# Optimization experiments

Measured on AMD Instinct MI355X. Metric: run time of the kernel, lower is better.

Reference implementation:

```python
import jax, jax.numpy as jnp
import numpy as np

HID = 256
HEADS = 8
DPH = HID // HEADS  # 32
N = 65536
E = 262144


def _ln(x, g, b):
    m = jnp.mean(x, axis=-1, keepdims=True)
    v = jnp.var(x, axis=-1, keepdims=True)
    return (x - m) * jax.lax.rsqrt(v + 1e-5) * g + b


def _gelu(x):
    return jax.nn.gelu(x, approximate=False)


def _mlp2(x, W1, b1, W2, b2, act):
    return act(x @ W1 + b1) @ W2 + b2


def setup_inputs() -> dict:
    key = jax.random.key(0)
    ks = jax.random.split(key, 32)
    d = {}
    d["x"] = jax.random.normal(ks[0], (N, HID), jnp.float32)
    d["edge_index"] = jax.random.randint(ks[1], (2, E), 0, N, dtype=jnp.int32)
    d["edge_attr"] = jax.random.normal(ks[2], (E, 7), jnp.float32)
    i = 3
    def p(shape, s=0.02):
        nonlocal i
        out = jax.random.normal(ks[i], shape, jnp.float32) * s
        i += 1
        return out
    for nm, (din, dh, do) in [("q", (2 * HID + 3, 2 * HID, HID)),
                              ("k", (2 * HID + 3, 2 * HID, HID)),
                              ("v", (2 * HID + 3, 2 * HID, HID)),
                              ("s", (4, 64, HEADS)),
                              ("f", (HID, 2 * HID, HID))]:
        d[nm + "W1"] = p((din, dh))
        d[nm + "b1"] = jnp.zeros((dh,), jnp.float32)
        d[nm + "W2"] = p((dh, do))
        d[nm + "b2"] = jnp.zeros((do,), jnp.float32)
    d["ln_g"] = jnp.ones((HID,), jnp.float32)
    d["ln_b"] = jnp.zeros((HID,), jnp.float32)
    d["rW"] = p((2 * HID, HID))
    d["rb"] = jnp.zeros((HID,), jnp.float32)
    return d


def reference(x, edge_index, edge_attr,
              qW1, qb1, qW2, qb2,
              kW1, kb1, kW2, kb2,
              vW1, vb1, vW2, vb2,
              sW1, sb1, sW2, sb2,
              ln_g, ln_b, rW, rb,
              fW1, fb1, fW2, fb2):
    n_nodes = x.shape[0]
    original_x = x
    residual = x
    xn = _ln(x, ln_g, ln_b)

    src = edge_index[0]
    dst = edge_index[1]
    # gather endpoint features, concat with molecular edge feats -> [E, 2*HID+3]
    comb = jnp.concatenate([xn[src], xn[dst], edge_attr[:, :3]], axis=1)

    Q = _mlp2(comb, qW1, qb1, qW2, qb2, _gelu).reshape(-1, HEADS, DPH)
    K = _mlp2(comb, kW1, kb1, kW2, kb2, _gelu).reshape(-1, HEADS, DPH)
    V = _mlp2(comb, vW1, vb1, vW2, vb2, _gelu).reshape(-1, HEADS, DPH)

    scale = jnp.sqrt(jnp.float32(DPH))
    scores = jnp.einsum('ehd,egd->ehg', Q, K) / scale  # [E, H, H]
    bias = _mlp2(edge_attr[:, 3:7], sW1, sb1, sW2, sb2, jax.nn.relu)[:, :, None]  # [E, H, 1]
    attn = jax.nn.softmax(scores + bias, axis=1)  # softmax over dim=1, as in torch code
    wv = jnp.einsum('ehg,egd->ehd', attn, V).reshape(-1, HID)  # [E, HID]

    # scatter-mean to target nodes (edge_index[1])
    sums = jax.ops.segment_sum(wv, dst, num_segments=n_nodes)
    cnt = jax.ops.segment_sum(jnp.ones((wv.shape[0],), wv.dtype), dst, num_segments=n_nodes)
    out = sums / jnp.maximum(cnt, 1.0)[:, None]

    x1 = residual + out
    fused = jnp.concatenate([x1, original_x], axis=-1)
    x2 = x1 + (fused @ rW + rb)
    x3 = x2 + _mlp2(_ln(x2, ln_g, ln_b), fW1, fb1, fW2, fb2, _gelu)
    return x3
```

## Files before the change

kernel.cpp:

```cpp
#include <hip/hip_runtime.h>

#define N_NODES 65536
#define N_EDGES 262144

typedef unsigned short u16;
typedef unsigned char u8;
typedef float f32x4 __attribute__((ext_vector_type(4)));
typedef _Float16 h2 __attribute__((ext_vector_type(2)));
typedef _Float16 v8h __attribute__((ext_vector_type(8)));

__device__ __forceinline__ u16 f2h(float f) {
  return __builtin_bit_cast(u16, (_Float16)f);
}
__device__ __forceinline__ u8 f2e5m2(float f) {
  _Float16 h = (_Float16)f;
  u16 hb = __builtin_bit_cast(u16, h);
  hb = (u16)(hb + 0x7F + ((hb >> 8) & 1));
  return (u8)(hb >> 8);
}
__device__ __forceinline__ void dec4(unsigned d, float* o) {
  o[0] = (float)__builtin_bit_cast(_Float16, (u16)((d << 8) & 0xFF00u));
  o[1] = (float)__builtin_bit_cast(_Float16, (u16)(d & 0xFF00u));
  o[2] = (float)__builtin_bit_cast(_Float16, (u16)((d >> 8) & 0xFF00u));
  o[3] = (float)__builtin_bit_cast(_Float16, (u16)((d >> 16) & 0xFF00u));
}
__device__ __forceinline__ h2 e5lo(unsigned d) {
  return __builtin_bit_cast(h2, __builtin_amdgcn_perm(d, 0u, 0x05000400u));
}
__device__ __forceinline__ h2 e5hi(unsigned d) {
  return __builtin_bit_cast(h2, __builtin_amdgcn_perm(d, 0u, 0x07000600u));
}
__device__ __forceinline__ float gelu_s(float x) {
  float e = __expf(1.702f * x);
  return x - __fdividef(x, e + 1.0f);
}
__device__ __forceinline__ float gelu_f(float x) {
  float y = 1.5957691216057308f * (x + 0.044715f * x * x * x);
  float e = __expf(y);
  return x - __fdividef(x, e + 1.0f);
}
__device__ __forceinline__ void gld16(const u16* g, u16* l) {
  __builtin_amdgcn_global_load_lds(
      (const __attribute__((address_space(1))) void*)g,
      (__attribute__((address_space(3))) void*)l, 16, 0, 0);
}

__global__ __launch_bounds__(256) void ln_kernel(const float* __restrict__ x,
                                                 const float* __restrict__ g,
                                                 const float* __restrict__ b,
                                                 u16* __restrict__ out) {
  int row = blockIdx.x * 4 + (threadIdx.x >> 6);
  int lane = threadIdx.x & 63;
  float4 v = ((const float4*)(x + (size_t)row * 256))[lane];
  float s = v.x + v.y + v.z + v.w;
  float s2 = v.x * v.x + v.y * v.y + v.z * v.z + v.w * v.w;
#pragma unroll
  for (int off = 1; off < 64; off <<= 1) {
    s += __shfl_xor(s, off, 64);
    s2 += __shfl_xor(s2, off, 64);
  }
  float mean = s * (1.0f / 256.0f);
  float var = s2 * (1.0f / 256.0f) - mean * mean;
  float rs = rsqrtf(var + 1e-5f);
  float4 gv = ((const float4*)g)[lane];
  float4 bv = ((const float4*)b)[lane];
  ushort4 o;
  o.x = f2h((v.x - mean) * rs * gv.x + bv.x);
  o.y = f2h((v.y - mean) * rs * gv.y + bv.y);
  o.z = f2h((v.z - mean) * rs * gv.z + bv.z);
  o.w = f2h((v.w - mean) * rs * gv.w + bv.w);
  *(ushort4*)(out + (size_t)row * 256 + lane * 4) = o;
}

template <typename Epi>
__global__ __launch_bounds__(256) void gemm_bt(const u16* __restrict__ A,
                                               const u16* __restrict__ BT,
                                               int K, Epi epi) {
  __shared__ __align__(16) u16 sA[128 * 48];
  __shared__ __align__(16) u16 sB[128 * 48];
  const int tm = blockIdx.x * 128, tn = blockIdx.y * 128;
  const int t = threadIdx.x;
  const int wave = t >> 6, lane = t & 63;
  const int lrow = lane & 15, quad = lane >> 4;
  const int wrow = (wave & 1) * 64, wcol = (wave >> 1) * 64;
  const int r = t >> 2, c = (t & 3) << 3;
  f32x4 acc[4][4];
  const f32x4 z = {0.f, 0.f, 0.f, 0.f};
#pragma unroll
  for (int i = 0; i < 4; ++i)
#pragma unroll
    for (int j = 0; j < 4; ++j) acc[i][j] = z;
  for (int k0 = 0; k0 < K; k0 += 32) {
    *(uint4*)&sA[r * 48 + c] = *(const uint4*)&A[(size_t)(tm + r) * K + k0 + c];
    *(uint4*)&sA[(r + 64) * 48 + c] = *(const uint4*)&A[(size_t)(tm + r + 64) * K + k0 + c];
    *(uint4*)&sB[r * 48 + c] = *(const uint4*)&BT[(size_t)(tn + r) * K + k0 + c];
    *(uint4*)&sB[(r + 64) * 48 + c] = *(const uint4*)&BT[(size_t)(tn + r + 64) * K + k0 + c];
    __syncthreads();
    v8h af[4], bfv[4];
#pragma unroll
    for (int i = 0; i < 4; ++i) af[i] = *(const v8h*)&sA[(wrow + i * 16 + lrow) * 48 + quad * 8];
#pragma unroll
    for (int j = 0; j < 4; ++j) bfv[j] = *(const v8h*)&sB[(wcol + j * 16 + lrow) * 48 + quad * 8];
#pragma unroll
    for (int i = 0; i < 4; ++i)
#pragma unroll
      for (int j = 0; j < 4; ++j)
        acc[i][j] = __builtin_amdgcn_mfma_f32_16x16x32_f16(af[i], bfv[j], acc[i][j], 0, 0, 0);
    __syncthreads();
  }
#pragma unroll
  for (int i = 0; i < 4; ++i)
#pragma unroll
    for (int j = 0; j < 4; ++j)
#pragma unroll
      for (int rg = 0; rg < 4; ++rg)
        epi(tm + wrow + i * 16 + quad * 4 + rg, tn + wcol + j * 16 + lrow, acc[i][j][rg]);
}

#define GEMM_DBUF(K_)                                                                    \
  const int t = threadIdx.x;                                                             \
  const int wave = t >> 6, lane = t & 63;                                                \
  const int lrow = lane & 15, quad = lane >> 4;                                          \
  const int wrow = (wave & 1) * 64, wcol = (wave >> 1) * 64;                             \
  const int sa0 = 2 * wave, sa1 = 2 * wave + 1;                                          \
  const u16* pa0 = A + (size_t)(tm + sa0 * 16 + lrow) * (K_) + quad * 8;                 \
  const u16* pa1 = A + (size_t)(tm + sa1 * 16 + lrow) * (K_) + quad * 8;                 \
  const u16* pb0 = BT + (size_t)(tn + sa0 * 16 + lrow) * (K_) + quad * 8;                \
  const u16* pb1 = BT + (size_t)(tn + sa1 * 16 + lrow) * (K_) + quad * 8;                \
  f32x4 acc[4][4];                                                                       \
  {                                                                                      \
    const f32x4 z = {0.f, 0.f, 0.f, 0.f};                                                \
    _Pragma("unroll") for (int i = 0; i < 4; ++i)                                        \
        _Pragma("unroll") for (int j = 0; j < 4; ++j) acc[i][j] = z;                     \
  }                                                                                      \
  gld16(pa0, &sAB[sa0 * 512]);                                                           \
  gld16(pa1, &sAB[sa1 * 512]);                                                           \
  gld16(pb0, &sAB[4096 + sa0 * 512]);                                                    \
  gld16(pb1, &sAB[4096 + sa1 * 512]);                                                    \
  pa0 += 32; pa1 += 32; pb0 += 32; pb1 += 32;                                            \
  __syncthreads();                                                                       \
  int cur = 0;                                                                           \
  _Pragma("unroll") for (int k0 = 32; k0 < (K_); k0 += 32) {                             \
    const int nxt = cur ^ 1;                                                             \
    gld16(pa0, &sAB[nxt * 8192 + sa0 * 512]);                                            \
    gld16(pa1, &sAB[nxt * 8192 + sa1 * 512]);                                            \
    gld16(pb0, &sAB[nxt * 8192 + 4096 + sa0 * 512]);                                     \
    gld16(pb1, &sAB[nxt * 8192 + 4096 + sa1 * 512]);                                     \
    pa0 += 32; pa1 += 32; pb0 += 32; pb1 += 32;                                          \
    v8h af[4], bfv[4];                                                                   \
    _Pragma("unroll") for (int i = 0; i < 4; ++i) af[i] =                                \
        *(const v8h*)&sAB[cur * 8192 + ((wave & 1) * 4 + i) * 512 + lane * 8];           \
    _Pragma("unroll") for (int j = 0; j < 4; ++j) bfv[j] =                               \
        *(const v8h*)&sAB[cur * 8192 + 4096 + ((wave >> 1) * 4 + j) * 512 + lane * 8];   \
    _Pragma("unroll") for (int i = 0; i < 4; ++i)                                        \
        _Pragma("unroll") for (int j = 0; j < 4; ++j) acc[i][j] =                        \
            __builtin_amdgcn_mfma_f32_16x16x32_f16(af[i], bfv[j], acc[i][j], 0, 0, 0);   \
    __syncthreads();                                                                     \
    cur = nxt;                                                                           \
  }                                                                                      \
  {                                                                                      \
    v8h af[4], bfv[4];                                                                   \
    _Pragma("unroll") for (int i = 0; i < 4; ++i) af[i] =                                \
        *(const v8h*)&sAB[cur * 8192 + ((wave & 1) * 4 + i) * 512 + lane * 8];           \
    _Pragma("unroll") for (int j = 0; j < 4; ++j) bfv[j] =                               \
        *(const v8h*)&sAB[cur * 8192 + 4096 + ((wave >> 1) * 4 + j) * 512 + lane * 8];   \
    _Pragma("unroll") for (int i = 0; i < 4; ++i)                                        \
        _Pragma("unroll") for (int j = 0; j < 4; ++j) acc[i][j] =                        \
            __builtin_amdgcn_mfma_f32_16x16x32_f16(af[i], bfv[j], acc[i][j], 0, 0, 0);   \
  }

__global__ __launch_bounds__(256) void gemm2_ab(const u16* __restrict__ A,
                                                const u16* __restrict__ BT,
                                                const float* __restrict__ b1cat,
                                                u8* __restrict__ out) {
  __shared__ __align__(16) u16 sAB[16384];
  const int bid = blockIdx.x;
  const int local = bid >> 3;
  const int mt = (bid & 7) * 64 + local / 24;
  const int nt = local % 24;
  const int tm = mt * 128, tn = nt * 128;
  GEMM_DBUF(256)
  __syncthreads();
  float bj[4];
#pragma unroll
  for (int j = 0; j < 4; ++j)
    bj[j] = (nt < 12) ? b1cat[tn + wcol + j * 16 + lrow] : 0.f;
  u8* sb = (u8*)sAB;
#pragma unroll
  for (int i = 0; i < 4; ++i)
#pragma unroll
    for (int j = 0; j < 4; ++j)
#pragma unroll
      for (int rg = 0; rg < 4; ++rg)
        sb[(wrow + i * 16 + quad * 4 + rg) * 136 + wcol + j * 16 + lrow] =
            f2e5m2(acc[i][j][rg] + bj[j]);
  __syncthreads();
  {
    int ir = t >> 1, sg = t & 1;
    const u8* srcp = &sb[ir * 136 + sg * 64];
    uint2* dstp = (uint2*)(out + (size_t)(tm + ir) * 3072 + tn + sg * 64);
#pragma unroll
    for (int q = 0; q < 8; ++q) dstp[q] = *(const uint2*)(srcp + q * 8);
  }
}

struct EpiX2 {
  float* x2;
  const float* x1;
  const float* rb;
  __device__ void operator()(int m, int n, float v) const {
    x2[(size_t)m * 256 + n] = v + rb[n] + x1[(size_t)m * 256 + n];
  }
};
struct EpiHf {
  u16* hf;
  const float* b1;
  __device__ void operator()(int m, int n, float v) const {
    hf[(size_t)m * 512 + n] = f2h(gelu_f(v + b1[n]));
  }
};
struct EpiOut {
  float* out;
  const float* b2;
  const float* x2;
  __device__ void operator()(int m, int n, float v) const {
    out[(size_t)m * 256 + n] = v + b2[n] + x2[(size_t)m * 256 + n];
  }
};

__global__ void prep_w1catT(u16* __restrict__ out, const float* __restrict__ qW1,
                            const float* __restrict__ kW1, const float* __restrict__ vW1) {
  int cIdx = blockIdx.x;
  int rIdx = threadIdx.x;
  int sec = cIdx >> 9;
  int h = cIdx & 511;
  int mlp = sec % 3;
  const float* W1 = (mlp == 0) ? qW1 : (mlp == 1) ? kW1 : vW1;
  int rowoff = (sec < 3) ? 0 : 256;
  out[(size_t)cIdx * 256 + rIdx] = f2h(W1[(size_t)(rowoff + rIdx) * 512 + h]);
}
__global__ void prep_w2T(u16* __restrict__ out, const float* __restrict__ qW2,
                         const float* __restrict__ kW2, const float* __restrict__ vW2) {
  int row = blockIdx.x;
  int m = row >> 8, n = row & 255;
  const float* W2 = (m == 0) ? qW2 : (m == 1) ? kW2 : vW2;
  for (int k = threadIdx.x; k < 512; k += 256)
    out[(size_t)row * 512 + k] = f2h(W2[(size_t)k * 256 + n]);
}
__global__ void transpose_cast(u16* __restrict__ out, const float* __restrict__ in, int K, int Nn) {
  int n = blockIdx.x;
  for (int k = threadIdx.x; k < K; k += blockDim.x)
    out[(size_t)n * K + k] = f2h(in[(size_t)k * Nn + n]);
}
__global__ void prep_w1e16(u16* __restrict__ out, const float* __restrict__ qW1,
                           const float* __restrict__ kW1, const float* __restrict__ vW1) {
  int b = blockIdx.x;
  int m = b / 3, r = b % 3;
  const float* W1 = (m == 0) ? qW1 : (m == 1) ? kW1 : vW1;
  out[(size_t)b * 512 + threadIdx.x] = f2h(W1[(size_t)(512 + r) * 512 + threadIdx.x]);
}
__global__ void prep_b1cat(float* __restrict__ out, const float* __restrict__ qb1,
                           const float* __restrict__ kb1, const float* __restrict__ vb1) {
  int idx = blockIdx.x * 256 + threadIdx.x;
  const float* b = (idx < 512) ? qb1 : (idx < 1024) ? kb1 : vb1;
  out[idx] = b[idx & 511];
}

__global__ __launch_bounds__(256) void bias_kernel(const float* __restrict__ eattr,
                                                   const float* __restrict__ sW1,
                                                   const float* __restrict__ sb1,
                                                   const float* __restrict__ sW2,
                                                   const float* __restrict__ sb2,
                                                   float* __restrict__ biasb) {
  int e = blockIdx.x * 256 + threadIdx.x;
  const float* ea = eattr + (size_t)e * 7;
  float a0 = ea[3], a1 = ea[4], a2 = ea[5], a3 = ea[6];
  float acc[8];
#pragma unroll
  for (int h = 0; h < 8; ++h) acc[h] = sb2[h];
#pragma unroll 4
  for (int j = 0; j < 64; ++j) {
    float zz = fmaxf(a0 * sW1[j] + a1 * sW1[64 + j] + a2 * sW1[128 + j] + a3 * sW1[192 + j] + sb1[j], 0.f);
#pragma unroll
    for (int h = 0; h < 8; ++h) acc[h] += zz * sW2[j * 8 + h];
  }
  float4* bp = (float4*)(biasb + (size_t)e * 8);
  float4 v0 = {acc[0], acc[1], acc[2], acc[3]};
  float4 v1 = {acc[4], acc[5], acc[6], acc[7]};
  bp[0] = v0;
  bp[1] = v1;
}

__global__ __launch_bounds__(256) void hist_kernel(const int* __restrict__ dst,
                                                   unsigned* __restrict__ cnt) {
  int e = blockIdx.x * 256 + threadIdx.x;
  atomicAdd(&cnt[dst[e]], 1u);
}
__global__ __launch_bounds__(1024) void scan_kernel(const unsigned* __restrict__ cnt,
                                                    unsigned* __restrict__ off,
                                                    unsigned* __restrict__ woff) {
  __shared__ unsigned s_part[1024];
  int t = threadIdx.x;
  unsigned local[64];
  unsigned run = 0;
  const uint4* cp = (const uint4*)(cnt + t * 64);
#pragma unroll
  for (int j = 0; j < 16; ++j) {
    uint4 v = cp[j];
    local[j * 4 + 0] = v.x; local[j * 4 + 1] = v.y;
    local[j * 4 + 2] = v.z; local[j * 4 + 3] = v.w;
  }
#pragma unroll
  for (int j = 0; j < 64; ++j) { unsigned c = local[j]; local[j] = run; run += c; }
  s_part[t] = run;
  __syncthreads();
  for (int d = 1; d < 1024; d <<= 1) {
    unsigned v = (t >= d) ? s_part[t - d] : 0u;
    __syncthreads();
    s_part[t] += v;
    __syncthreads();
  }
  unsigned base = (t == 0) ? 0u : s_part[t - 1];
  for (int j = 0; j < 64; ++j) {
    unsigned o = base + local[j];
    off[t * 64 + j] = o;
    woff[t * 64 + j] = o;
  }
}
__global__ __launch_bounds__(256) void scatter_ids(const int* __restrict__ dst,
                                                   unsigned* __restrict__ woff,
                                                   unsigned* __restrict__ eid) {
  int e = blockIdx.x * 256 + threadIdx.x;
  unsigned pos = atomicAdd(&woff[dst[e]], 1u);
  eid[pos] = (unsigned)e;
}

__global__ __launch_bounds__(256, 4) void qkv_attn(
    const int* __restrict__ eidx, const float* __restrict__ eattr,
    const unsigned* __restrict__ eid,
    const u8* __restrict__ AB, const u16* __restrict__ W2T, const u16* __restrict__ w1e16,
    const float* __restrict__ qb2, const float* __restrict__ kb2, const float* __restrict__ vb2,
    const float* __restrict__ biasb, u8* __restrict__ wv) {
  __shared__ __align__(16) u8 sQ[32][784];
  __shared__ __align__(16) u8 sRaw[8704];
  __shared__ int s_src[32], s_dst[32];
  __shared__ unsigned s_eid[32];
  __shared__ __align__(16) float s_ea[32][4];
  u16(*sH)[136] = (u16(*)[136])sRaw;
  float(*sS)[8][8] = (float(*)[8][8])sRaw;
  const int t = threadIdx.x;
  const int e0 = blockIdx.x * 32;
  if (t < 32) {
    unsigned e = eid[e0 + t];
    s_eid[t] = e;
    s_src[t] = eidx[e];
    s_dst[t] = eidx[N_EDGES + e];
    const float* ea = eattr + (size_t)e * 7;
    s_ea[t][0] = ea[0]; s_ea[t][1] = ea[1]; s_ea[t][2] = ea[2];
  }
  __syncthreads();
  const int i = t & 31, seg = t >> 5;
  const int lane = t & 63, wave = t >> 6;
  const int lrow = lane & 15, quad = lane >> 4;
  const int wcol = wave * 64;
  h2 ea0h, ea1h, ea2h;
  ea0h[0] = ea0h[1] = (_Float16)s_ea[i][0];
  ea1h[0] = ea1h[1] = (_Float16)s_ea[i][1];
  ea2h[0] = ea2h[1] = (_Float16)s_ea[i][2];
  const u8* ABs = AB + (size_t)s_src[i] * 3072 + seg * 16;
  const u8* ABd = AB + (size_t)s_dst[i] * 3072 + 1536 + seg * 16;
  uint4 cs, cd, ns, nd;
  cs = *(const uint4*)(ABs);
  cd = *(const uint4*)(ABd);
  f32x4 acc[2][4];
#pragma unroll 1
  for (int c = 0; c < 12; ++c) {
    const int m = c >> 2, q = c & 3;
    const int k0 = q * 128;
    if (q == 0) {
      const f32x4 z = {0.f, 0.f, 0.f, 0.f};
#pragma unroll
      for (int i2 = 0; i2 < 2; ++i2)
#pragma unroll
        for (int j = 0; j < 4; ++j) acc[i2][j] = z;
    }
    if (c < 11) {
      const int cn = c + 1;
      ns = *(const uint4*)(ABs + (cn >> 2) * 512 + (cn & 3) * 128);
      nd = *(const uint4*)(ABd + (cn >> 2) * 512 + (cn & 3) * 128);
    }
    {
      const unsigned* w32 = (const unsigned*)(w1e16 + (size_t)m * 1536);
      alignas(16) unsigned sd[4], dd[4];
      *(uint4*)&sd[0] = cs;
      *(uint4*)&dd[0] = cd;
      const int cp0 = (k0 + seg * 16) >> 1;
      alignas(16) unsigned hout[8];
#pragma unroll
      for (int d = 0; d < 4; ++d) {
        int cp = cp0 + d * 2;
        h2 slo = e5lo(sd[d]) + e5lo(dd[d]);
        h2 shi = e5hi(sd[d]) + e5hi(dd[d]);
        slo += ea0h * __builtin_bit_cast(h2, w32[cp]);
        shi += ea0h * __builtin_bit_cast(h2, w32[cp + 1]);
        slo += ea1h * __builtin_bit_cast(h2, w32[256 + cp]);
        shi += ea1h * __builtin_bit_cast(h2, w32[256 + cp + 1]);
        slo += ea2h * __builtin_bit_cast(h2, w32[512 + cp]);
        shi += ea2h * __builtin_bit_cast(h2, w32[512 + cp + 1]);
        float g0 = gelu_s((float)slo[0]), g1 = gelu_s((float)slo[1]);
        float g2 = gelu_s((float)shi[0]), g3 = gelu_s((float)shi[1]);
        hout[d * 2] = (unsigned)f2h(g0) | ((unsigned)f2h(g1) << 16);
        hout[d * 2 + 1] = (unsigned)f2h(g2) | ((unsigned)f2h(g3) << 16);
      }
      uint4* hp = (uint4*)&sH[i][seg * 16];
      hp[0] = *(const uint4*)&hout[0];
      hp[1] = *(const uint4*)&hout[4];
    }
    __syncthreads();
    {
      const u16* Wm = W2T + (size_t)(m * 256 + wcol) * 512;
#pragma unroll
      for (int ks = 0; ks < 4; ++ks) {
        int kk = ks * 32;
        v8h a0 = *(const v8h*)&sH[lrow][kk + quad * 8];
        v8h a1 = *(const v8h*)&sH[16 + lrow][kk + quad * 8];
#pragma unroll
        for (int j = 0; j < 4; ++j) {
          v8h b = *(const v8h*)&Wm[(size_t)(j * 16 + lrow) * 512 + k0 + kk + quad * 8];
          acc[0][j] = __builtin_amdgcn_mfma_f32_16x16x32_f16(a0, b, acc[0][j], 0, 0, 0);
          acc[1][j] = __builtin_amdgcn_mfma_f32_16x16x32_f16(a1, b, acc[1][j], 0, 0, 0);
        }
      }
    }
    __syncthreads();
    cs = ns;
    cd = nd;
    if (q == 3) {
      const float* b2 = (m == 0) ? qb2 : (m == 1) ? kb2 : vb2;
#pragma unroll
      for (int i2 = 0; i2 < 2; ++i2)
#pragma unroll
        for (int j = 0; j < 4; ++j)
#pragma unroll
          for (int rg = 0; rg < 4; ++rg) {
            int row = i2 * 16 + quad * 4 + rg;
            int col = wcol + j * 16 + lrow;
            sQ[row][m * 256 + col] = f2e5m2(acc[i2][j][rg] + b2[col]);
          }
    }
  }
  __syncthreads();
  const int hh = t & 7, ii = t >> 3;
  {
    alignas(16) unsigned qd[8];
    *(uint4*)&qd[0] = *(const uint4*)&sQ[ii][hh * 32];
    *(uint4*)&qd[4] = *(const uint4*)&sQ[ii][hh * 32 + 16];
    h2 qh[16];
#pragma unroll
    for (int d = 0; d < 8; ++d) { qh[d * 2] = e5lo(qd[d]); qh[d * 2 + 1] = e5hi(qd[d]); }
    float bias = biasb[(size_t)s_eid[ii] * 8 + hh];
    float sc[8];
#pragma unroll
    for (int g = 0; g < 8; ++g) {
      alignas(16) unsigned kd[8];
      *(uint4*)&kd[0] = *(const uint4*)&sQ[ii][256 + g * 32];
      *(uint4*)&kd[4] = *(const uint4*)&sQ[ii][256 + g * 32 + 16];
      h2 acc2;
      acc2[0] = acc2[1] = (_Float16)0.f;
#pragma unroll
      for (int d = 0; d < 8; ++d) {
        acc2 += qh[d * 2] * e5lo(kd[d]);
        acc2 += qh[d * 2 + 1] * e5hi(kd[d]);
      }
      sc[g] = (float)acc2[0] + (float)acc2[1];
    }
#pragma unroll
    for (int g = 0; g < 8; ++g) sS[ii][hh][g] = sc[g] * 0.17677669529663687f + bias;
  }
  __syncthreads();
  {
    const int g = hh;
    float mx = -1e30f;
#pragma unroll
    for (int h2i = 0; h2i < 8; ++h2i) mx = fmaxf(mx, sS[ii][h2i][g]);
    float ev[8], ssum = 0.f;
#pragma unroll
    for (int h2i = 0; h2i < 8; ++h2i) {
      ev[h2i] = __expf(sS[ii][h2i][g] - mx);
      ssum += ev[h2i];
    }
    float inv = 1.0f / ssum;
#pragma unroll
    for (int h2i = 0; h2i < 8; ++h2i) sS[ii][h2i][g] = ev[h2i] * inv;
  }
  __syncthreads();
  {
    h2 va[16];
#pragma unroll
    for (int u = 0; u < 16; ++u) va[u][0] = va[u][1] = (_Float16)0.f;
#pragma unroll
    for (int g = 0; g < 8; ++g) {
      float at = sS[ii][hh][g];
      h2 at2;
      at2[0] = at2[1] = (_Float16)at;
      alignas(16) unsigned vd[8];
      *(uint4*)&vd[0] = *(const uint4*)&sQ[ii][512 + g * 32];
      *(uint4*)&vd[4] = *(const uint4*)&sQ[ii][512 + g * 32 + 16];
#pragma unroll
      for (int d = 0; d < 8; ++d) {
        va[d * 2] += at2 * e5lo(vd[d]);
        va[d * 2 + 1] += at2 * e5hi(vd[d]);
      }
    }
    alignas(16) unsigned od[8];
#pragma unroll
    for (int p = 0; p < 8; ++p) {
      unsigned a = __builtin_bit_cast(unsigned, va[p * 2]) + 0x00800080u;
      unsigned b = __builtin_bit_cast(unsigned, va[p * 2 + 1]) + 0x00800080u;
      od[p] = __builtin_amdgcn_perm(b, a, 0x07050301u);
    }
    u8* dp = wv + (size_t)(e0 + ii) * 256 + hh * 32;
    *(uint4*)dp = *(const uint4*)&od[0];
    *(uint4*)(dp + 16) = *(const uint4*)&od[4];
  }
}

__global__ __launch_bounds__(256) void node_gather(const unsigned* __restrict__ off,
                                                   const unsigned* __restrict__ cnt,
                                                   const u8* __restrict__ wv,
                                                   const float* __restrict__ x,
                                                   float* __restrict__ x1,
                                                   u16* __restrict__ X1cat) {
  int n = blockIdx.x * 4 + (threadIdx.x >> 6);
  int lane = threadIdx.x & 63;
  unsigned st = off[n], c = cnt[n];
  float a0 = 0.f, a1 = 0.f, a2 = 0.f, a3 = 0.f;
  for (unsigned j = 0; j < c; ++j) {
    unsigned d = *(const unsigned*)(wv + (size_t)(st + j) * 256 + lane * 4);
    float f[4];
    dec4(d, f);
    a0 += f[0]; a1 += f[1]; a2 += f[2]; a3 += f[3];
  }
  float inv = 1.0f / fmaxf((float)c, 1.0f);
  float4 xv = *(const float4*)(x + (size_t)n * 256 + lane * 4);
  float4 x1v = {xv.x + a0 * inv, xv.y + a1 * inv, xv.z + a2 * inv, xv.w + a3 * inv};
  *(float4*)(x1 + (size_t)n * 256 + lane * 4) = x1v;
  ushort4 a, bq;
  a.x = f2h(x1v.x); a.y = f2h(x1v.y); a.z = f2h(x1v.z); a.w = f2h(x1v.w);
  bq.x = f2h(xv.x); bq.y = f2h(xv.y); bq.z = f2h(xv.z); bq.w = f2h(xv.w);
  *(ushort4*)(X1cat + (size_t)n * 512 + lane * 4) = a;
  *(ushort4*)(X1cat + (size_t)n * 512 + 256 + lane * 4) = bq;
}

extern "C" void kernel_launch(void* const* d_in, const int* in_sizes, int n_in,
                              void* d_out, int out_size, void* d_ws, size_t ws_size,
                              hipStream_t stream) {
  const float* x = (const float*)d_in[0];
  const int* eidx = (const int*)d_in[1];
  const float* eattr = (const float*)d_in[2];
  const float* qW1 = (const float*)d_in[3];
  const float* qb1 = (const float*)d_in[4];
  const float* qW2 = (const float*)d_in[5];
  const float* qb2 = (const float*)d_in[6];
  const float* kW1 = (const float*)d_in[7];
  const float* kb1 = (const float*)d_in[8];
  const float* kW2 = (const float*)d_in[9];
  const float* kb2 = (const float*)d_in[10];
  const float* vW1 = (const float*)d_in[11];
  const float* vb1 = (const float*)d_in[12];
  const float* vW2 = (const float*)d_in[13];
  const float* vb2 = (const float*)d_in[14];
  const float* sW1 = (const float*)d_in[15];
  const float* sb1 = (const float*)d_in[16];
  const float* sW2 = (const float*)d_in[17];
  const float* sb2 = (const float*)d_in[18];
  const float* fW1 = (const float*)d_in[19];
  const float* fb1 = (const float*)d_in[20];
  const float* fW2 = (const float*)d_in[21];
  const float* fb2 = (const float*)d_in[22];
  const float* lng = (const float*)d_in[23];
  const float* lnb = (const float*)d_in[24];
  const float* rW = (const float*)d_in[25];
  const float* rb = (const float*)d_in[26];

  const size_t N = N_NODES;
  char* ws = (char*)d_ws;
  size_t off_b = 0;
  auto alloc = [&](size_t bytes) {
    void* p = ws + off_b;
    off_b = (off_b + bytes + 255) & ~(size_t)255;
    return p;
  };
  u16* W1catT = (u16*)alloc((size_t)3072 * 256 * 2);
  u16* W2T = (u16*)alloc((size_t)768 * 512 * 2);
  u16* rWT = (u16*)alloc((size_t)256 * 512 * 2);
  u16* fW1T = (u16*)alloc((size_t)512 * 256 * 2);
  u16* fW2T = (u16*)alloc((size_t)256 * 512 * 2);
  u16* w1e16 = (u16*)alloc((size_t)9 * 512 * 2);
  float* b1cat = (float*)alloc((size_t)1536 * 4);
  unsigned* cnt = (unsigned*)alloc(N * 4);
  unsigned* offs = (unsigned*)alloc(N * 4);
  unsigned* woff = (unsigned*)alloc(N * 4);
  unsigned* eid = (unsigned*)alloc((size_t)N_EDGES * 4);
  float* biasb = (float*)alloc((size_t)N_EDGES * 8 * 4);
  u8* AB = (u8*)alloc(N * 3072);
  u16* xn = (u16*)d_out;
  u8* wv = (u8*)d_out;
  float* x1 = (float*)AB;
  u16* X1cat = (u16*)(AB + (size_t)67108864);
  float* x2 = (float*)(AB + (size_t)134217728);
  u16* xn2 = (u16*)AB;
  u16* Hf = (u16*)(AB + (size_t)33554432);

  hipMemsetAsync(cnt, 0, N * 4, stream);
  hist_kernel<<<N_EDGES / 256, 256, 0, stream>>>(eidx + N_EDGES, cnt);
  scan_kernel<<<1, 1024, 0, stream>>>(cnt, offs, woff);
  scatter_ids<<<N_EDGES / 256, 256, 0, stream>>>(eidx + N_EDGES, woff, eid);
  prep_w1catT<<<3072, 256, 0, stream>>>(W1catT, qW1, kW1, vW1);
  prep_w2T<<<768, 256, 0, stream>>>(W2T, qW2, kW2, vW2);
  prep_w1e16<<<9, 512, 0, stream>>>(w1e16, qW1, kW1, vW1);
  prep_b1cat<<<6, 256, 0, stream>>>(b1cat, qb1, kb1, vb1);
  transpose_cast<<<256, 256, 0, stream>>>(rWT, rW, 512, 256);
  transpose_cast<<<512, 256, 0, stream>>>(fW1T, fW1, 256, 512);
  transpose_cast<<<256, 256, 0, stream>>>(fW2T, fW2, 512, 256);
  bias_kernel<<<N_EDGES / 256, 256, 0, stream>>>(eattr, sW1, sb1, sW2, sb2, biasb);

  ln_kernel<<<N_NODES / 4, 256, 0, stream>>>(x, lng, lnb, xn);
  gemm2_ab<<<12288, 256, 0, stream>>>(xn, W1catT, b1cat, AB);
  qkv_attn<<<N_EDGES / 32, 256, 0, stream>>>(eidx, eattr, eid, AB, W2T, w1e16,
                                             qb2, kb2, vb2, biasb, wv);
  node_gather<<<N_NODES / 4, 256, 0, stream>>>(offs, cnt, wv, x, x1, X1cat);
  gemm_bt<<<dim3(N_NODES / 128, 2), 256, 0, stream>>>(X1cat, rWT, 512, EpiX2{x2, x1, rb});
  ln_kernel<<<N_NODES / 4, 256, 0, stream>>>(x2, lng, lnb, xn2);
  gemm_bt<<<dim3(N_NODES / 128, 4), 256, 0, stream>>>(xn2, fW1T, 256, EpiHf{Hf, fb1});
  gemm_bt<<<dim3(N_NODES / 128, 2), 256, 0, stream>>>(Hf, fW2T, 512, EpiOut{(float*)d_out, fb2, x2});
}
```

Measured before the change: 1.592 ms.

## Double-buffer hidden tile in qkv_attn to overlap GELU assembly with MFMA

After: 1.630 ms. +2.4%, slower.

```diff
diff --git a/kernel.cpp b/kernel.cpp
--- a/kernel.cpp
+++ b/kernel.cpp
@@ -335,18 +335,17 @@
   eid[pos] = (unsigned)e;
 }
 
-__global__ __launch_bounds__(256, 4) void qkv_attn(
+__global__ __launch_bounds__(256, 3) void qkv_attn(
     const int* __restrict__ eidx, const float* __restrict__ eattr,
     const unsigned* __restrict__ eid,
     const u8* __restrict__ AB, const u16* __restrict__ W2T, const u16* __restrict__ w1e16,
     const float* __restrict__ qb2, const float* __restrict__ kb2, const float* __restrict__ vb2,
     const float* __restrict__ biasb, u8* __restrict__ wv) {
   __shared__ __align__(16) u8 sQ[32][784];
-  __shared__ __align__(16) u8 sRaw[8704];
+  __shared__ __align__(16) u8 sRaw[17408];
   __shared__ int s_src[32], s_dst[32];
   __shared__ unsigned s_eid[32];
   __shared__ __align__(16) float s_ea[32][4];
-  u16(*sH)[136] = (u16(*)[136])sRaw;
   float(*sS)[8][8] = (float(*)[8][8])sRaw;
   const int t = threadIdx.x;
   const int e0 = blockIdx.x * 32;
@@ -369,14 +368,59 @@
   ea2h[0] = ea2h[1] = (_Float16)s_ea[i][2];
   const u8* ABs = AB + (size_t)s_src[i] * 3072 + seg * 16;
   const u8* ABd = AB + (size_t)s_dst[i] * 3072 + 1536 + seg * 16;
-  uint4 cs, cd, ns, nd;
-  cs = *(const uint4*)(ABs);
-  cd = *(const uint4*)(ABd);
+  u16* sH0 = (u16*)sRaw;
+  u16* sH1 = (u16*)(sRaw + 8704);
+
+  auto assemble = [&](int cn, uint4 gs, uint4 gd, u16* sHw) {
+    const int mq = cn >> 2, qq = cn & 3;
+    const int k0a = qq * 128;
+    const unsigned* w32 = (const unsigned*)(w1e16 + (size_t)mq * 1536);
+    alignas(16) unsigned sd[4], dd[4];
+    *(uint4*)&sd[0] = gs;
+    *(uint4*)&dd[0] = gd;
+    const int cp0 = (k0a + seg * 16) >> 1;
+    alignas(16) unsigned hout[8];
+#pragma unroll
+    for (int d = 0; d < 4; ++d) {
+      int cp = cp0 + d * 2;
+      h2 slo = e5lo(sd[d]) + e5lo(dd[d]);
+      h2 shi = e5hi(sd[d]) + e5hi(dd[d]);
+      slo += ea0h * __builtin_bit_cast(h2, w32[cp]);
+      shi += ea0h * __builtin_bit_cast(h2, w32[cp + 1]);
+      slo += ea1h * __builtin_bit_cast(h2, w32[256 + cp]);
+      shi += ea1h * __builtin_bit_cast(h2, w32[256 + cp + 1]);
+      slo += ea2h * __builtin_bit_cast(h2, w32[512 + cp]);
+      shi += ea2h * __builtin_bit_cast(h2, w32[512 + cp + 1]);
+      float g0 = gelu_s((float)slo[0]), g1 = gelu_s((float)slo[1]);
+      float g2 = gelu_s((float)shi[0]), g3 = gelu_s((float)shi[1]);
+      hout[d * 2] = (unsigned)f2h(g0) | ((unsigned)f2h(g1) << 16);
+      hout[d * 2 + 1] = (unsigned)f2h(g2) | ((unsigned)f2h(g3) << 16);
+    }
+    uint4* hp = (uint4*)(sHw + i * 136 + seg * 16);
+    hp[0] = *(const uint4*)&hout[0];
+    hp[1] = *(const uint4*)&hout[4];
+  };
+
+  uint4 c0s = *(const uint4*)(ABs);
+  uint4 c0d = *(const uint4*)(ABd);
+  uint4 g1s = *(const uint4*)(ABs + 128);
+  uint4 g1d = *(const uint4*)(ABd + 128);
+  assemble(0, c0s, c0d, sH0);
+  __syncthreads();
+  u16* sHr = sH0;
+  u16* sHw = sH1;
   f32x4 acc[2][4];
 #pragma unroll 1
   for (int c = 0; c < 12; ++c) {
     const int m = c >> 2, q = c & 3;
     const int k0 = q * 128;
+    uint4 g2s = g1s, g2d = g1d;
+    if (c + 2 < 12) {
+      const int cn = c + 2;
+      g2s = *(const uint4*)(ABs + (cn >> 2) * 512 + (cn & 3) * 128);
+      g2d = *(const uint4*)(ABd + (cn >> 2) * 512 + (cn & 3) * 128);
+    }
+    if (c + 1 < 12) assemble(c + 1, g1s, g1d, sHw);
     if (q == 0) {
       const f32x4 z = {0.f, 0.f, 0.f, 0.f};
 #pragma unroll
@@ -384,46 +428,13 @@
 #pragma unroll
         for (int j = 0; j < 4; ++j) acc[i2][j] = z;
     }
-    if (c < 11) {
-      const int cn = c + 1;
-      ns = *(const uint4*)(ABs + (cn >> 2) * 512 + (cn & 3) * 128);
-      nd = *(const uint4*)(ABd + (cn >> 2) * 512 + (cn & 3) * 128);
-    }
-    {
-      const unsigned* w32 = (const unsigned*)(w1e16 + (size_t)m * 1536);
-      alignas(16) unsigned sd[4], dd[4];
-      *(uint4*)&sd[0] = cs;
-      *(uint4*)&dd[0] = cd;
-      const int cp0 = (k0 + seg * 16) >> 1;
-      alignas(16) unsigned hout[8];
-#pragma unroll
-      for (int d = 0; d < 4; ++d) {
-        int cp = cp0 + d * 2;
-        h2 slo = e5lo(sd[d]) + e5lo(dd[d]);
-        h2 shi = e5hi(sd[d]) + e5hi(dd[d]);
-        slo += ea0h * __builtin_bit_cast(h2, w32[cp]);
-        shi += ea0h * __builtin_bit_cast(h2, w32[cp + 1]);
-        slo += ea1h * __builtin_bit_cast(h2, w32[256 + cp]);
-        shi += ea1h * __builtin_bit_cast(h2, w32[256 + cp + 1]);
-        slo += ea2h * __builtin_bit_cast(h2, w32[512 + cp]);
-        shi += ea2h * __builtin_bit_cast(h2, w32[512 + cp + 1]);
-        float g0 = gelu_s((float)slo[0]), g1 = gelu_s((float)slo[1]);
-        float g2 = gelu_s((float)shi[0]), g3 = gelu_s((float)shi[1]);
-        hout[d * 2] = (unsigned)f2h(g0) | ((unsigned)f2h(g1) << 16);
-        hout[d * 2 + 1] = (unsigned)f2h(g2) | ((unsigned)f2h(g3) << 16);
-      }
-      uint4* hp = (uint4*)&sH[i][seg * 16];
-      hp[0] = *(const uint4*)&hout[0];
-      hp[1] = *(const uint4*)&hout[4];
-    }
-    __syncthreads();
     {
       const u16* Wm = W2T + (size_t)(m * 256 + wcol) * 512;
 #pragma unroll
       for (int ks = 0; ks < 4; ++ks) {
         int kk = ks * 32;
-        v8h a0 = *(const v8h*)&sH[lrow][kk + quad * 8];
-        v8h a1 = *(const v8h*)&sH[16 + lrow][kk + quad * 8];
+        v8h a0 = *(const v8h*)(sHr + lrow * 136 + kk + quad * 8);
+        v8h a1 = *(const v8h*)(sHr + (16 + lrow) * 136 + kk + quad * 8);
 #pragma unroll
         for (int j = 0; j < 4; ++j) {
           v8h b = *(const v8h*)&Wm[(size_t)(j * 16 + lrow) * 512 + k0 + kk + quad * 8];
@@ -432,9 +443,6 @@
         }
       }
     }
-    __syncthreads();
-    cs = ns;
-    cd = nd;
     if (q == 3) {
       const float* b2 = (m == 0) ? qb2 : (m == 1) ? kb2 : vb2;
 #pragma unroll
@@ -448,8 +456,10 @@
             sQ[row][m * 256 + col] = f2e5m2(acc[i2][j][rg] + b2[col]);
           }
     }
-  }
-  __syncthreads();
+    __syncthreads();
+    u16* tmp = sHr; sHr = sHw; sHw = tmp;
+    g1s = g2s; g1d = g2d;
+  }
   const int hh = t & 7, ii = t >> 3;
   {
     alignas(16) unsigned qd[8];
```
